# Kernel optimization log

Measured on AMD Instinct MI355X. Metric: run time of the kernel, lower is better.

Reference implementation:

```python
import jax, jax.numpy as jnp
import numpy as np

CYCLE = 24  # cycle_length


def setup_inputs() -> dict:
    key = jax.random.key(0)
    ks = jax.random.split(key, 10)
    B, T, C, E, L, Ty = 32, 2048, 128, 256, 512, 128
    timesteps = jax.random.uniform(ks[0], (B, T), dtype=jnp.float32) * 240.0  # 10 daily cycles
    X = jax.random.normal(ks[1], (B, T, C), dtype=jnp.float32)
    M = jax.random.randint(ks[2], (B, T, C), 0, 2, dtype=jnp.int32)  # observation mask
    y_times = jax.random.uniform(ks[3], (B, Ty), dtype=jnp.float32) * 240.0
    # params: time_linear (Linear(1,E) -> weight [E], bias [E])
    time_w = jax.random.normal(ks[4], (E,), dtype=jnp.float32) * 0.1
    time_b = jax.random.normal(ks[5], (E,), dtype=jnp.float32) * 0.1
    channel_embed = jax.random.normal(ks[6], (C, E), dtype=jnp.float32)
    dec_w1 = jax.random.normal(ks[7], (E, L), dtype=jnp.float32) * (1.0 / np.sqrt(E))
    dec_b1 = jnp.zeros((L,), dtype=jnp.float32)
    dec_w2 = jax.random.normal(ks[8], (L, C), dtype=jnp.float32) * (1.0 / np.sqrt(L))
    dec_b2 = jnp.zeros((C,), dtype=jnp.float32)
    return {"timesteps": timesteps, "X": X, "M": M, "y_times": y_times,
            "time_w": time_w, "time_b": time_b, "channel_embed": channel_embed,
            "dec_w1": dec_w1, "dec_b1": dec_b1, "dec_w2": dec_w2, "dec_b2": dec_b2}


def reference(timesteps, X, M, y_times, time_w, time_b, channel_embed,
              dec_w1, dec_b1, dec_w2, dec_b2):
    # --- _get_cycle: phase-bucket masked mean, vectorized as one-hot segmented reduce ---
    phases = jnp.floor(timesteps).astype(jnp.int32) % CYCLE            # [B,T]
    onehot = jax.nn.one_hot(phases, CYCLE, dtype=X.dtype)              # [B,T,P]
    Mf = M.astype(X.dtype)
    sum_p = jnp.einsum('btp,btc->bpc', onehot, X * Mf)                 # [B,P,C]
    cnt_p = jnp.maximum(jnp.einsum('btp,btc->bpc', onehot, Mf), 1.0)   # clamp(min=1)
    c_base = sum_p / cnt_p                                             # [B,P,C]
    # (X - c_in is computed in the original but never used downstream)

    # --- learn_time: Linear(1,E) + sin, then pooled mean over T*C of (Et + Ec) ---
    E_lin = timesteps[..., None] * time_w + time_b                     # [B,T,E]
    Et = E_lin + jnp.sin(E_lin)                                        # [B,T,E]
    # mean over flattened (T,C) of Et[b,t,None,:] + Ec[None,None,c,:]
    pooled = Et.mean(axis=1) + channel_embed.mean(axis=0)              # [B,E]

    # --- decoder MLP ---
    h = jax.nn.relu(pooled @ dec_w1 + dec_b1)                          # [B,L]
    Y = h @ dec_w2 + dec_b2                                            # [B,C]

    # --- residual cycle add-back at forecast times ---
    phases_out = jnp.floor(y_times).astype(jnp.int32) % CYCLE          # [B,Ty]
    c_fut = jnp.take_along_axis(c_base, phases_out[:, :, None], axis=1)  # [B,Ty,C]
    return Y[:, None, :] + c_fut                                       # [B,Ty,C]
```

## Files before the change

### kernel.cpp

```cpp
#include <hip/hip_runtime.h>
#include <math.h>

#define BB 32
#define TT 2048
#define CC 128
#define EE 256
#define LL 512
#define TYY 128
#define PP 24
#define KS 8
#define KT 256
#define NST 8

#define WS_PBUF  0
#define WS_TPART 1572864
#define WS_CEM   1703936
#define WS_H     1704192

typedef __attribute__((ext_vector_type(8))) short bf16x8;
typedef __attribute__((ext_vector_type(4))) float f32x4;

__device__ __forceinline__ unsigned int pack_bf2(float a, float b) {
    unsigned int ua = __float_as_uint(a);
    unsigned int ub = __float_as_uint(b);
    ua = (ua + 0x7FFFu + ((ua >> 16) & 1u)) >> 16;
    ub = (ub + 0x7FFFu + ((ub >> 16) & 1u)) & 0xFFFF0000u;
    return ua | ub;
}

__global__ __launch_bounds__(512) void k_main(const float* __restrict__ ts,
                                              const float* __restrict__ X,
                                              const int*   __restrict__ M,
                                              const float* __restrict__ tw,
                                              const float* __restrict__ tbias,
                                              const float* __restrict__ ce,
                                              float* __restrict__ pbuf,
                                              float* __restrict__ tpart,
                                              float* __restrict__ cemean) {
    __shared__ unsigned short wbuf[2][256 * 32];
    __shared__ float s_ts[KT];
    __shared__ int   s_p[KT];

    const int tid = threadIdx.x;
    const int blk = blockIdx.x;

    if (blk == BB * KS) {
        if (tid < EE) {
            float s = 0.0f;
#pragma unroll 16
            for (int c = 0; c < CC; ++c) s += ce[c * EE + tid];
            cemean[tid] = s * (1.0f / CC);
        }
        return;
    }

    const int b   = blk >> 3;
    const int ks  = blk & 7;
    const int tB  = ks * KT;

    if (tid < KT) {
        const float v = ts[b * TT + tB + tid];
        s_ts[tid] = v;
        s_p[tid] = ((int)floorf(v)) % PP;
    }

    const int jq = tid & 31;
    const int tp = tid >> 5;
    const int slot = tp ^ ((jq & 3) << 2);
    float4 xq[2][2]; int4 mq[2][2];

    const int wv   = tid >> 6;
    const int lane = tid & 63;
    const int mt   = wv & 1;
    const int jt0  = (wv >> 1) * 4;
    const int mrow = mt * 16 + (lane & 15);
    const int kg   = lane >> 4;
    const int k0   = kg * 8;
    const int n16  = lane & 15;

    const int se = tid & 255;
    const int sh = tid >> 8;
    const float sw = tw[se];
    const float sb = tbias[se];
    float sacc = 0.0f;

    f32x4 acc[4];
#pragma unroll
    for (int jl = 0; jl < 4; ++jl) acc[jl] = (f32x4){0.f, 0.f, 0.f, 0.f};

    auto LOADS = [&](int s) {
        const int pr = s & 1;
#pragma unroll
        for (int it = 0; it < 2; ++it) {
            const int t = tB + s * 32 + tp * 2 + it;
            const long r0 = ((long)(b * TT + t)) * CC + jq * 4;
            xq[pr][it] = *(const float4*)(X + r0);
            mq[pr][it] = *(const int4*)(M + r0);
        }
    };

    auto WRITES = [&](int s) {
        const int pr = s & 1;
        unsigned int* wb = (unsigned int*)wbuf[pr];
        const float4 x0 = xq[pr][0], x1 = xq[pr][1];
        const int4   m0 = mq[pr][0], m1 = mq[pr][1];
        wb[(4 * jq + 0) * 16 + slot] = pack_bf2(m0.x ? x0.x : 0.f, m1.x ? x1.x : 0.f);
        wb[(4 * jq + 1) * 16 + slot] = pack_bf2(m0.y ? x0.y : 0.f, m1.y ? x1.y : 0.f);
        wb[(4 * jq + 2) * 16 + slot] = pack_bf2(m0.z ? x0.z : 0.f, m1.z ? x1.z : 0.f);
        wb[(4 * jq + 3) * 16 + slot] = pack_bf2(m0.w ? x0.w : 0.f, m1.w ? x1.w : 0.f);
        wb[(128 + 4 * jq + 0) * 16 + slot] = (m0.x ? 0x3F80u : 0u) | (m1.x ? 0x3F800000u : 0u);
        wb[(128 + 4 * jq + 1) * 16 + slot] = (m0.y ? 0x3F80u : 0u) | (m1.y ? 0x3F800000u : 0u);
        wb[(128 + 4 * jq + 2) * 16 + slot] = (m0.z ? 0x3F80u : 0u) | (m1.z ? 0x3F800000u : 0u);
        wb[(128 + 4 * jq + 3) * 16 + slot] = (m0.w ? 0x3F80u : 0u) | (m1.w ? 0x3F800000u : 0u);
    };

    auto SINC = [&](int s) {
#pragma unroll
        for (int j = 0; j < 16; ++j) {
            const float v = fmaf(s_ts[s * 32 + sh * 16 + j], sw, sb);
            sacc += v + __sinf(v);
        }
    };

    LOADS(0);
    WRITES(0);
    LOADS(1);
    __syncthreads();

    unsigned int au_all[NST][4];
#pragma unroll
    for (int s = 0; s < NST; ++s) {
        const int tb0 = s * 32 + k0;
        const int4 pA = *(const int4*)&s_p[tb0];
        const int4 pB = *(const int4*)&s_p[tb0 + 4];
        au_all[s][0] = (pA.x == mrow ? 0x3F80u : 0u) | (pA.y == mrow ? 0x3F800000u : 0u);
        au_all[s][1] = (pA.z == mrow ? 0x3F80u : 0u) | (pA.w == mrow ? 0x3F800000u : 0u);
        au_all[s][2] = (pB.x == mrow ? 0x3F80u : 0u) | (pB.y == mrow ? 0x3F800000u : 0u);
        au_all[s][3] = (pB.z == mrow ? 0x3F80u : 0u) | (pB.w == mrow ? 0x3F800000u : 0u);
    }

#pragma unroll
    for (int s = 0; s < NST; ++s) {
        if (s > 0) {
            asm volatile("s_waitcnt lgkmcnt(0)" ::: "memory");
            __builtin_amdgcn_s_barrier();
        }
        if (s + 2 < NST) LOADS(s + 2);
        {
            union { unsigned int u[4]; bf16x8 v; } au;
            au.u[0] = au_all[s][0]; au.u[1] = au_all[s][1];
            au.u[2] = au_all[s][2]; au.u[3] = au_all[s][3];
#pragma unroll
            for (int jl = 0; jl < 4; ++jl) {
                const int jrow = (jt0 + jl) * 16 + n16;
                const int bx = kg ^ ((jrow >> 2) & 3);
                const bf16x8 bv = *(const bf16x8*)&wbuf[s & 1][jrow * 32 + bx * 8];
                acc[jl] = __builtin_amdgcn_mfma_f32_16x16x32_bf16(au.v, bv, acc[jl], 0, 0, 0);
            }
        }
        SINC(s);
        if (s + 1 < NST) WRITES(s + 1);
    }

    tpart[((b * KS + ks) * 2 + sh) * EE + se] = sacc;

    float* pbb = pbuf + ((long)blk) * PP * 256;
#pragma unroll
    for (int jl = 0; jl < 4; ++jl) {
#pragma unroll
        for (int r = 0; r < 4; ++r) {
            const int p = mt * 16 + kg * 4 + r;
            if (p < PP)
                pbb[p * 256 + (jt0 + jl) * 16 + n16] = acc[jl][r];
        }
    }
}

__global__ __launch_bounds__(256) void k_hid(const float* __restrict__ tpart,
                                             const float* __restrict__ cemean,
                                             const float* __restrict__ w1,
                                             const float* __restrict__ b1,
                                             float* __restrict__ hbuf) {
    __shared__ float s_pool[EE];
    __shared__ float s_hp[256];
    const int b = blockIdx.x >> 3;
    const int q = blockIdx.x & 7;
    const int tid = threadIdx.x;

    {
        float sp = 0.0f;
#pragma unroll
        for (int k = 0; k < KS * 2; ++k) sp += tpart[(b * KS * 2 + k) * EE + tid];
        s_pool[tid] = sp * (1.0f / TT) + cemean[tid];
    }
    __syncthreads();

    const int l = q * 64 + (tid & 63);
    const int eq = tid >> 6;
    float ha = 0.0f;
#pragma unroll 16
    for (int e = eq * 64; e < eq * 64 + 64; ++e)
        ha = fmaf(s_pool[e], w1[e * LL + l], ha);
    s_hp[tid] = ha;
    __syncthreads();
    if (tid < 64)
        hbuf[b * LL + q * 64 + tid] =
            fmaxf(b1[q * 64 + tid] + s_hp[tid] + s_hp[tid + 64]
                  + s_hp[tid + 128] + s_hp[tid + 192], 0.0f);
}

__global__ __launch_bounds__(256) void k_out(const float* __restrict__ hbuf,
                                             const float* __restrict__ w2,
                                             const float* __restrict__ b2,
                                             const float* __restrict__ pbuf,
                                             const float* __restrict__ yt,
                                             float* __restrict__ out) {
    __shared__ float s_h[LL];
    __shared__ float s_yp[256];
    __shared__ float s_y[16];
    __shared__ float s_cb[PP * 16];
    __shared__ int   s_ph[TYY];
    const int b  = blockIdx.x >> 3;
    const int co = blockIdx.x & 7;
    const int tid = threadIdx.x;

    for (int i = tid; i < LL; i += 256) s_h[i] = hbuf[b * LL + i];
    if (tid < TYY) {
        const float v = yt[b * TYY + tid];
        int p = ((int)floorf(v)) % PP; if (p < 0) p += PP;
        s_ph[tid] = p;
    }
    __syncthreads();

    {
        const int c16 = tid & 15;
        const int lg = tid >> 4;
        float y = 0.0f;
#pragma unroll 8
        for (int l = lg * 32; l < lg * 32 + 32; ++l)
            y = fmaf(s_h[l], w2[l * CC + co * 16 + c16], y);
        s_yp[tid] = y;
    }
    for (int i = tid; i < PP * 16; i += 256) {
        const int p = i >> 4;
        const int c = co * 16 + (i & 15);
        float s = 0.0f, n = 0.0f;
#pragma unroll
        for (int k = 0; k < KS; ++k) {
            const float* pb = pbuf + ((long)(b * KS + k)) * PP * 256 + p * 256;
            s += pb[c];
            n += pb[128 + c];
        }
        s_cb[i] = s / fmaxf(n, 1.0f);
    }
    __syncthreads();
    if (tid < 16) {
        float yy = b2[co * 16 + tid];
#pragma unroll
        for (int g = 0; g < 16; ++g) yy += s_yp[tid + 16 * g];
        s_y[tid] = yy;
    }
    __syncthreads();

    for (int i = tid; i < TYY * 16; i += 256) {
        const int ty = i >> 4;
        const int ci = i & 15;
        out[((long)(b * TYY + ty)) * CC + co * 16 + ci] =
            s_y[ci] + s_cb[s_ph[ty] * 16 + ci];
    }
}

extern "C" void kernel_launch(void* const* d_in, const int* in_sizes, int n_in,
                              void* d_out, int out_size, void* d_ws, size_t ws_size,
                              hipStream_t stream) {
    const float* ts   = (const float*)d_in[0];
    const float* X    = (const float*)d_in[1];
    const int*   M    = (const int*)  d_in[2];
    const float* yt   = (const float*)d_in[3];
    const float* tw   = (const float*)d_in[4];
    const float* tb   = (const float*)d_in[5];
    const float* ce   = (const float*)d_in[6];
    const float* w1   = (const float*)d_in[7];
    const float* b1   = (const float*)d_in[8];
    const float* w2   = (const float*)d_in[9];
    const float* b2   = (const float*)d_in[10];
    float* out = (float*)d_out;

    float* ws     = (float*)d_ws;
    float* pbuf   = ws + WS_PBUF;
    float* tpart  = ws + WS_TPART;
    float* cemean = ws + WS_CEM;
    float* hbuf   = ws + WS_H;

    k_main<<<BB * KS + 1, 512, 0, stream>>>(ts, X, M, tw, tb, ce, pbuf, tpart, cemean);
    k_hid<<<BB * 8, 256, 0, stream>>>(tpart, cemean, w1, b1, hbuf);
    k_out<<<BB * 8, 256, 0, stream>>>(hbuf, w2, b2, pbuf, yt, out);
}
```

Before: 28.30 us.

## Fuse hidden-layer and output kernels into a single tail kernel

Merges k_hid and k_out into one k_tail kernel with 512 threads. Each block now computes the full 512-wide hidden vector itself, so the hbuf round-trip through global memory and one kernel launch go away. The cost is that each of the 8 blocks per batch repeats the whole E×L first-layer matvec, an 8× increase in w1 reads and FLOPs for that stage. The w1 reads should mostly hit in L2.

New measurement: 31.00 us. 1.1x slower.

```diff
diff --git a/kernel.cpp b/kernel.cpp
--- a/kernel.cpp
+++ b/kernel.cpp
@@ -15,7 +15,6 @@
 #define WS_PBUF  0
 #define WS_TPART 1572864
 #define WS_CEM   1703936
-#define WS_H     1704192
 
 typedef __attribute__((ext_vector_type(8))) short bf16x8;
 typedef __attribute__((ext_vector_type(4))) float f32x4;
@@ -176,47 +175,18 @@
     }
 }
 
-__global__ __launch_bounds__(256) void k_hid(const float* __restrict__ tpart,
-                                             const float* __restrict__ cemean,
-                                             const float* __restrict__ w1,
-                                             const float* __restrict__ b1,
-                                             float* __restrict__ hbuf) {
+__global__ __launch_bounds__(512) void k_tail(const float* __restrict__ tpart,
+                                              const float* __restrict__ cemean,
+                                              const float* __restrict__ w1,
+                                              const float* __restrict__ b1,
+                                              const float* __restrict__ w2,
+                                              const float* __restrict__ b2,
+                                              const float* __restrict__ pbuf,
+                                              const float* __restrict__ yt,
+                                              float* __restrict__ out) {
     __shared__ float s_pool[EE];
-    __shared__ float s_hp[256];
-    const int b = blockIdx.x >> 3;
-    const int q = blockIdx.x & 7;
-    const int tid = threadIdx.x;
-
-    {
-        float sp = 0.0f;
-#pragma unroll
-        for (int k = 0; k < KS * 2; ++k) sp += tpart[(b * KS * 2 + k) * EE + tid];
-        s_pool[tid] = sp * (1.0f / TT) + cemean[tid];
-    }
-    __syncthreads();
-
-    const int l = q * 64 + (tid & 63);
-    const int eq = tid >> 6;
-    float ha = 0.0f;
-#pragma unroll 16
-    for (int e = eq * 64; e < eq * 64 + 64; ++e)
-        ha = fmaf(s_pool[e], w1[e * LL + l], ha);
-    s_hp[tid] = ha;
-    __syncthreads();
-    if (tid < 64)
-        hbuf[b * LL + q * 64 + tid] =
-            fmaxf(b1[q * 64 + tid] + s_hp[tid] + s_hp[tid + 64]
-                  + s_hp[tid + 128] + s_hp[tid + 192], 0.0f);
-}
-
-__global__ __launch_bounds__(256) void k_out(const float* __restrict__ hbuf,
-                                             const float* __restrict__ w2,
-                                             const float* __restrict__ b2,
-                                             const float* __restrict__ pbuf,
-                                             const float* __restrict__ yt,
-                                             float* __restrict__ out) {
     __shared__ float s_h[LL];
-    __shared__ float s_yp[256];
+    __shared__ float s_yp[512];
     __shared__ float s_y[16];
     __shared__ float s_cb[PP * 16];
     __shared__ int   s_ph[TYY];
@@ -224,45 +194,65 @@
     const int co = blockIdx.x & 7;
     const int tid = threadIdx.x;
 
-    for (int i = tid; i < LL; i += 256) s_h[i] = hbuf[b * LL + i];
+    {
+        const int se = tid & 255;
+        const int half = tid >> 8;
+        float sp = 0.0f;
+#pragma unroll
+        for (int k = half * 8; k < half * 8 + 8; ++k)
+            sp += tpart[(b * 16 + k) * EE + se];
+        s_yp[tid] = sp;
+    }
     if (tid < TYY) {
         const float v = yt[b * TYY + tid];
         int p = ((int)floorf(v)) % PP; if (p < 0) p += PP;
         s_ph[tid] = p;
     }
     __syncthreads();
+    if (tid < EE)
+        s_pool[tid] = (s_yp[tid] + s_yp[tid + 256]) * (1.0f / TT) + cemean[tid];
+    __syncthreads();
+
+    {
+        float ha = b1[tid];
+#pragma unroll 16
+        for (int e = 0; e < EE; ++e)
+            ha = fmaf(s_pool[e], w1[e * LL + tid], ha);
+        s_h[tid] = fmaxf(ha, 0.0f);
+    }
+    for (int i = tid; i < PP * 16; i += 512) {
+        const int p = i >> 4;
+        const int c = co * 16 + (i & 15);
+        float s = 0.0f, n = 0.0f;
+#pragma unroll
+        for (int k = 0; k < KS; ++k) {
+            const float* pb = pbuf + ((long)(b * KS + k)) * PP * 256 + p * 256;
+            s += pb[c];
+            n += pb[128 + c];
+        }
+        s_cb[i] = s / fmaxf(n, 1.0f);
+    }
+    __syncthreads();
 
     {
         const int c16 = tid & 15;
         const int lg = tid >> 4;
         float y = 0.0f;
-#pragma unroll 8
-        for (int l = lg * 32; l < lg * 32 + 32; ++l)
+#pragma unroll
+        for (int l = lg * 16; l < lg * 16 + 16; ++l)
             y = fmaf(s_h[l], w2[l * CC + co * 16 + c16], y);
         s_yp[tid] = y;
     }
-    for (int i = tid; i < PP * 16; i += 256) {
-        const int p = i >> 4;
-        const int c = co * 16 + (i & 15);
-        float s = 0.0f, n = 0.0f;
-#pragma unroll
-        for (int k = 0; k < KS; ++k) {
-            const float* pb = pbuf + ((long)(b * KS + k)) * PP * 256 + p * 256;
-            s += pb[c];
-            n += pb[128 + c];
-        }
-        s_cb[i] = s / fmaxf(n, 1.0f);
-    }
     __syncthreads();
     if (tid < 16) {
         float yy = b2[co * 16 + tid];
 #pragma unroll
-        for (int g = 0; g < 16; ++g) yy += s_yp[tid + 16 * g];
+        for (int g = 0; g < 32; ++g) yy += s_yp[tid + 16 * g];
         s_y[tid] = yy;
     }
     __syncthreads();
 
-    for (int i = tid; i < TYY * 16; i += 256) {
+    for (int i = tid; i < TYY * 16; i += 512) {
         const int ty = i >> 4;
         const int ci = i & 15;
         out[((long)(b * TYY + ty)) * CC + co * 16 + ci] =
@@ -290,9 +280,7 @@
     float* pbuf   = ws + WS_PBUF;
     float* tpart  = ws + WS_TPART;
     float* cemean = ws + WS_CEM;
-    float* hbuf   = ws + WS_H;
 
     k_main<<<BB * KS + 1, 512, 0, stream>>>(ts, X, M, tw, tb, ce, pbuf, tpart, cemean);
-    k_hid<<<BB * 8, 256, 0, stream>>>(tpart, cemean, w1, b1, hbuf);
-    k_out<<<BB * 8, 256, 0, stream>>>(hbuf, w2, b2, pbuf, yt, out);
-}
+    k_tail<<<BB * 8, 512, 0, stream>>>(tpart, cemean, w1, b1, w2, b2, pbuf, yt, out);
+}
```
